# Performance work log

Hardware: AMD Instinct MI355X
Metric: run time of the kernel (lower is better)

## Reference

```python
import jax, jax.numpy as jnp
import numpy as np

B, D, L = 16, 256, 200
T = 1000   # max_frame_length
K = 3      # kernel_size
DW, DC = 4, 2


def setup_inputs() -> dict:
    key = jax.random.key(0)
    ks = jax.random.split(key, 16)
    plen = jax.random.randint(ks[0], (B,), 150, L + 1)
    pm = jnp.arange(L)[None, :] < plen[:, None]              # (B,L) True=valid
    phoneme_mask = pm[:, None, :]                            # (B,1,L)
    durations = jax.random.uniform(ks[1], (B, L), minval=1.0, maxval=8.0) * pm
    phoneme = jax.random.normal(ks[2], (B, D, L), dtype=jnp.float32)
    s = 0.05
    params = {
        'Wpw': jax.random.normal(ks[3], (D, D)) * s, 'bpw': jnp.zeros((D,)),
        'Cw': jax.random.normal(ks[4], (8, D, K)) * s, 'cbw': jnp.zeros((8,)),
        'Mw': jax.random.normal(ks[5], (10, DW)) * s, 'mbw': jnp.zeros((DW,)),
        'Lw': jax.random.normal(ks[6], (DW * D, D)) * s, 'lbw': jnp.zeros((D,)),
        'Wpc': jax.random.normal(ks[7], (D, D)) * s, 'bpc': jnp.zeros((D,)),
        'Cc': jax.random.normal(ks[8], (8, D, K)) * s, 'cbc': jnp.zeros((8,)),
        'Mc': jax.random.normal(ks[9], (10, DC)) * s, 'mbc': jnp.zeros((DC,)),
        'Lc': jax.random.normal(ks[10], (DW * DC, D)) * s, 'lbc': jnp.zeros((D,)),
        'Wo': jax.random.normal(ks[11], (D, 2 * D)) * s, 'bo': jnp.zeros((2 * D,)),
    }
    return {'durations': durations, 'phoneme': phoneme, 'phoneme_mask': phoneme_mask, **params}


def _conv_swish(x, W1, b1, Ck, cb, pm):
    # 1x1 conv (proj) then kernel-K 'same' conv then SiLU; mask padded phones
    h = jnp.einsum('od,bdl->bol', W1, x) + b1[None, :, None]
    h = jax.lax.conv_general_dilated(h, Ck, (1,), 'SAME',
                                     dimension_numbers=('NCH', 'OIH', 'NCH')) + cb[None, :, None]
    h = jax.nn.silu(h)
    h = jnp.where(pm[:, None, :], h, 0.0)
    return h.transpose(0, 2, 1)  # (B, L, 8)


def _mlp(S, E, h, M, mb):
    # concat start/end boundary scalars with per-phone conv features -> (B,T,L,10)
    feat = jnp.concatenate([S[..., None], E[..., None],
                            jnp.broadcast_to(h[:, None], (B, T, L, 8))], axis=-1)
    return jax.nn.silu(feat @ M + mb)


def _forward(durations, phoneme, phoneme_mask, Wpw, bpw, Cw, cbw, Mw, mbw, Lw, lbw,
             Wpc, bpc, Cc, cbc, Mc, mbc, Lc, lbc, Wo, bo):
    pm = phoneme_mask[:, 0, :]                                          # (B,L)
    frame_lengths = jnp.clip(jnp.round(durations.sum(-1)).astype(jnp.int32), 0, T)
    frame_mask = jnp.arange(T)[None, :] < frame_lengths[:, None]        # (B,T)
    attn_mask = frame_mask[:, :, None] & pm[:, None, :]                 # (B,T,L)
    sd = jnp.cumsum(durations, axis=-1)                                 # (B,L)
    sk = sd - durations
    t = jnp.arange(1, T + 1, dtype=durations.dtype)
    S = jnp.where(attn_mask, t[None, :, None] - sk[:, None, :], 0.0)    # (B,T,L)
    E = jnp.where(attn_mask, (sd - sk)[:, None, :], 0.0)                # (B,T,L)

    h_w = _conv_swish(phoneme, Wpw, bpw, Cw, cbw, pm)
    w = _mlp(S, E, h_w, Mw, mbw)                                        # (B,T,L,DW)
    w = jnp.where(pm[:, None, :, None], w, -jnp.inf)
    w = jax.nn.softmax(w, axis=2)                                       # softmax over phones
    w = jnp.where(frame_mask[:, :, None, None], w, 0.0)

    h_c = _conv_swish(phoneme, Wpc, bpc, Cc, cbc, pm)
    c = _mlp(S, E, h_c, Mc, mbc)                                        # (B,T,L,DC)

    wh = jnp.einsum('btlq,bdl->btqd', w, phoneme).reshape(B, T, DW * D) @ Lw + lbw
    wc = jnp.einsum('btlq,btlp->btqp', w, c).reshape(B, T, DW * DC) @ Lc + lbc
    whc = jnp.where(frame_mask[..., None], wh + wc, 0.0)                # (B,T,D)
    out = (whc @ Wo + bo).transpose(0, 2, 1)                            # (B,2D,T)
    return out, frame_mask, frame_lengths, w.transpose(0, 3, 1, 2)


def reference(durations, phoneme, phoneme_mask, Wpw, bpw, Cw, cbw, Mw, mbw, Lw, lbw,
              Wpc, bpc, Cc, cbc, Mc, mbc, Lc, lbc, Wo, bo):
    out, frame_mask, frame_lengths, w = _forward(
        durations, phoneme, phoneme_mask, Wpw, bpw, Cw, cbw, Mw, mbw, Lw, lbw,
        Wpc, bpc, Cc, cbc, Mc, mbc, Lc, lbc, Wo, bo)
    mean, log_std = jnp.split(out, 2, axis=1)                           # (B,D,T) each
    return (mean, log_std, frame_mask, frame_lengths, w)
```

## Files before the change

kernel.cpp:

```cpp
#include <hip/hip_runtime.h>
#include <hip/hip_bf16.h>
#include <math.h>

#define NB 16
#define ND 256
#define NL 200
#define NT 1000

typedef unsigned short ushort_t;
typedef __bf16 bf16x8 __attribute__((ext_vector_type(8)));
typedef float f32x4 __attribute__((ext_vector_type(4)));

#define OFF_FL    4981936u
#define OFF_GT    11535552u
#define OFF_WOT   15221952u
#define OFF_BASE  15287488u

__device__ __forceinline__ float silu_f(float x){ return x / (1.f + __expf(-x)); }
__device__ __forceinline__ ushort_t f2bf(float x){
  __hip_bfloat16 h = __float2bfloat16(x);
  return *(ushort_t*)&h;
}

__global__ __launch_bounds__(256, 2) void k_A(
    const float* __restrict__ dur, const float* __restrict__ ph,
    const float* __restrict__ Wp_w, const float* __restrict__ C_w, const float* __restrict__ bp_w,
    const float* __restrict__ Wp_c, const float* __restrict__ C_c, const float* __restrict__ bp_c,
    const float* __restrict__ Wo, const float* __restrict__ Lw,
    const float* __restrict__ cbw, const float* __restrict__ cbc,
    const float* __restrict__ Mw, const float* __restrict__ mbw,
    const float* __restrict__ Mc, const float* __restrict__ mbc,
    int* __restrict__ fl_ws, float* __restrict__ o_fm, float* __restrict__ o_fl,
    ushort_t* __restrict__ WoT, float4* __restrict__ base,
    ushort_t* __restrict__ Gt)
{
  __shared__ __align__(16) unsigned char smem[69632];
  int bid = blockIdx.x, tid = threadIdx.x;

  if (bid < 256){
    int r = bid;
    int b = r >> 4, x = r & 15;
    if (x >= 13){
      int l0 = 208 + (x - 13)*16;
      if (tid < 32)
        base[((size_t)(b*256 + l0 + (tid >> 1)))*2 + (tid & 1)] = make_float4(0,0,0,0);
      return;
    }
    float* sdur = (float*)smem;
    float* ssk  = sdur + 256;
    float (*phs)[256] = (float (*)[256])(ssk + 256);
    float (*Uw)[20] = (float (*)[20])((float*)phs + 18*256);
    float (*Uc)[20] = Uw + 256;
    float (*sh)[17] = (float (*)[17])((float*)Uc + 256*20);
    int l0 = x*16;

    if (tid < NL) sdur[tid] = dur[b*NL + tid];
    __syncthreads();
    if (tid == 0){
      float run = 0.f;
      for (int l = 0; l < NL; ++l){ ssk[l] = run; run += sdur[l]; }
    }
    {
      int d = tid;
      const float* pr = ph + ((size_t)b*ND + d)*NL;
      #pragma unroll
      for (int j = 0; j < 18; ++j){
        int l = l0 - 1 + j;
        phs[j][d] = (l >= 0 && l < NL) ? pr[l] : 0.f;
      }
    }
    __syncthreads();
    {
      int i = tid;
      float uw[18], uc[18];
      float bw = bp_w[i], bc = bp_c[i];
      #pragma unroll
      for (int j = 0; j < 18; ++j){ uw[j] = bw; uc[j] = bc; }
      const float4* wr = (const float4*)(Wp_w + (size_t)i*ND);
      const float4* cr = (const float4*)(Wp_c + (size_t)i*ND);
      for (int d4 = 0; d4 < 64; ++d4){
        float4 a = wr[d4], c = cr[d4];
        #pragma unroll
        for (int j = 0; j < 18; ++j){
          float4 p = *(const float4*)&phs[j][d4*4];
          uw[j] += a.x*p.x + a.y*p.y + a.z*p.z + a.w*p.w;
          uc[j] += c.x*p.x + c.y*p.y + c.z*p.z + c.w*p.w;
        }
      }
      #pragma unroll
      for (int j = 0; j < 18; ++j){
        int l = l0 - 1 + j;
        bool pad = (l < 0 || l >= NL);
        Uw[i][j] = pad ? 0.f : uw[j];
        Uc[i][j] = pad ? 0.f : uc[j];
      }
    }
    __syncthreads();
    {
      int lu = tid >> 4, u = tid & 15;
      int l = l0 + lu;
      float h = 0.f;
      if (l < NL){
        int branch = u >> 3, oc = u & 7;
        float (*U)[20] = branch ? Uc : Uw;
        const float* C = branch ? C_c : C_w;
        float val = (branch ? cbc : cbw)[oc];
        #pragma unroll 4
        for (int i = 0; i < ND; ++i){
          const float* cc = C + ((size_t)oc*ND + i)*3;
          val += cc[0]*U[i][lu] + cc[1]*U[i][lu + 1] + cc[2]*U[i][lu + 2];
        }
        float pm = (sdur[l] > 0.5f) ? 1.f : 0.f;
        h = silu_f(val) * pm;
      }
      sh[lu][u] = h;
    }
    __syncthreads();
    if (tid < 16){
      int ll = x*16 + tid;
      float4 o0 = make_float4(0,0,0,0);
      float4 o1 = make_float4(0,0,0,0);
      if (ll < NL){
        float dl  = sdur[ll];
        float pm  = (dl > 0.5f) ? 1.f : 0.f;
        float skl = ssk[ll];
        float c1[4], c2[2];
        #pragma unroll
        for (int q = 0; q < 4; ++q) c1[q] = mbw[q] + dl*Mw[4 + q] - skl*Mw[q];
        #pragma unroll
        for (int p = 0; p < 2; ++p) c2[p] = mbc[p] + dl*Mc[2 + p] - skl*Mc[p];
        #pragma unroll
        for (int j = 0; j < 8; ++j){
          float hwv = sh[tid][j], hcv = sh[tid][8 + j];
          #pragma unroll
          for (int q = 0; q < 4; ++q) c1[q] += hwv*Mw[(2 + j)*4 + q];
          #pragma unroll
          for (int p = 0; p < 2; ++p) c2[p] += hcv*Mc[(2 + j)*2 + p];
        }
        o0 = make_float4(c1[0], c1[1], c1[2], c1[3]);
        o1 = make_float4(c2[0], c2[1], pm, 0.f);
      }
      base[((size_t)(b*256 + ll))*2 + 0] = o0;
      base[((size_t)(b*256 + ll))*2 + 1] = o1;
    }
  } else if (bid < 512){
    int r = bid - 256;
    int xb = r & 1, yb = (r >> 1) & 1, bq = r >> 2;
    int b = bq >> 2, q = bq & 3;
    int m0 = yb * 128;
    int n0 = xb * 128;
    int lane = tid & 63, wave = tid >> 6;
    int wm = wave >> 1, wn = wave & 1;
    int col = lane & 15, kg4 = lane >> 4;
    ushort_t (*Asub)[136] = (ushort_t (*)[136])smem;
    ushort_t (*Bsub)[136] = (ushort_t (*)[136])(smem + 34816);
    int na = lane*2;

    f32x4 acc[4][4] = {};
    for (int kh = 0; kh < 2; ++kh){
      int d0 = kh*128;
      for (int rep = 0; rep < 32; ++rep){
        int dk = wave*32 + rep;
        float2 v = *(const float2*)(Lw + ((size_t)(q*256 + d0 + dk))*ND + m0 + na);
        Asub[na    ][dk] = f2bf(v.x);
        Asub[na + 1][dk] = f2bf(v.y);
      }
      for (int rep = 0; rep < 32; ++rep){
        int dk = wave*32 + rep;
        int l = n0 + na;
        float2 v; v.x = 0.f; v.y = 0.f;
        if (l < NL)
          v = *(const float2*)(ph + ((size_t)b*ND + d0 + dk)*NL + l);
        Bsub[na    ][dk] = f2bf(v.x);
        Bsub[na + 1][dk] = f2bf(v.y);
      }
      __syncthreads();
      for (int kt = 0; kt < 4; ++kt){
        int k0 = kt*32;
        bf16x8 afr[4], bfr[4];
        #pragma unroll
        for (int i = 0; i < 4; ++i)
          afr[i] = *(const bf16x8*)&Asub[wm*64 + i*16 + col][k0 + kg4*8];
        #pragma unroll
        for (int j = 0; j < 4; ++j)
          bfr[j] = *(const bf16x8*)&Bsub[wn*64 + j*16 + col][k0 + kg4*8];
        #pragma unroll
        for (int i = 0; i < 4; ++i)
          #pragma unroll
          for (int j = 0; j < 4; ++j)
            acc[i][j] = __builtin_amdgcn_mfma_f32_16x16x32_bf16(afr[i], bfr[j], acc[i][j], 0, 0, 0);
      }
      __syncthreads();
    }
    ushort_t (*st2)[136] = Asub;
    int rq = lane >> 4;
    #pragma unroll
    for (int i = 0; i < 4; ++i){
      #pragma unroll
      for (int rr = 0; rr < 4; ++rr){
        int rl = wm*64 + i*16 + rq*4 + rr;
        #pragma unroll
        for (int j = 0; j < 4; ++j){
          int cl = wn*64 + j*16 + col;
          st2[rl][cl] = f2bf(acc[i][j][rr]);
        }
      }
    }
    __syncthreads();
    #pragma unroll
    for (int rep = 0; rep < 8; ++rep){
      int row = rep*16 + (tid >> 4);
      int ch  = tid & 15;
      int l   = n0 + ch*8;
      if (l < NL){
        int n = m0 + row;
        *(uint4*)(Gt + ((size_t)(b*ND + n))*800 + q*NL + l) = *(const uint4*)&st2[row][ch*8];
      }
    }
  } else if (bid < 528){
    int b = bid - 512;
    float* sdur = (float*)smem;
    int* sfl = (int*)(sdur + 256);
    if (tid < NL) sdur[tid] = dur[b*NL + tid];
    __syncthreads();
    if (tid == 0){
      float run = 0.f;
      for (int l = 0; l < NL; ++l) run += sdur[l];
      int fl = (int)rintf(run);
      fl = fl < 0 ? 0 : (fl > NT ? NT : fl);
      sfl[0] = fl; fl_ws[b] = fl; o_fl[b] = (float)fl;
    }
    __syncthreads();
    int flv = sfl[0];
    for (int t = tid; t < NT; t += 256) o_fm[b*NT + t] = (t < flv) ? 1.f : 0.f;
  } else {
    int base_id = (bid - 528)*256 + tid;
    #pragma unroll
    for (int rep = 0; rep < 4; ++rep){
      int gid = rep*32768 + base_id;
      int n = gid >> 8, k = gid & 255;
      WoT[gid] = f2bf(Wo[(size_t)k*512 + n]);
    }
  }
}

#define AP 808
#define TT 64
__global__ __launch_bounds__(1024, 4) void k_wv_fused(
    const float4* __restrict__ base,
    const int* __restrict__ fl_ws,
    const float* __restrict__ Mw, const float* __restrict__ Mc,
    const ushort_t* __restrict__ Gt,
    const float* __restrict__ Lc,
    const float* __restrict__ lbc,
    const float* __restrict__ lbw,
    const ushort_t* __restrict__ WoT,
    const float* __restrict__ bo,
    float* __restrict__ wout,
    float* __restrict__ o_mean, float* __restrict__ o_lstd)
{
  __shared__ ushort_t As[TT*AP];
  __shared__ float    wcs[TT][8];
  int b = blockIdx.x;
  int m0 = blockIdx.y * TT;
  int tid = threadIdx.x, lane = tid & 63, wave = tid >> 6;
  int col = lane & 15, kg4 = lane >> 4;
  int fl = fl_ws[b];

  if (fl <= m0){
    for (int idx = tid; idx < TT*4*50; idx += 1024){
      int tl = idx / 200;
      int rqs = idx - tl*200;
      int q = rqs / 50, seg = rqs - q*50;
      int t = m0 + tl;
      if (t < NT)
        *(float4*)&wout[(((size_t)(b*4 + q))*NT + t)*NL + seg*4] = make_float4(0,0,0,0);
    }
    for (int idx = tid; idx < 512*16; idx += 1024){
      int s = idx >> 4, j = idx & 15;
      int t0 = m0 + j*4;
      if (t0 + 3 < NT){
        float v = bo[s];
        float4 v4 = make_float4(v, v, v, v);
        if (s < ND) *(float4*)&o_mean[((size_t)b*ND + s)*NT + t0] = v4;
        else        *(float4*)&o_lstd[((size_t)b*ND + (s - ND))*NT + t0] = v4;
      }
    }
    return;
  }

  int l0 = lane*4;
  bool lv = (l0 < NL);

  #pragma unroll
  for (int s = 0; s < 4; ++s){
    int tl = wave*4 + s, t = m0 + tl;
    if (t < fl) continue;
    for (int k = l0; k < 800; k += 256){
      uint2 zz2; zz2.x = 0u; zz2.y = 0u;
      *(uint2*)&As[tl*AP + k] = zz2;
    }
    if (lane < 8) wcs[tl][lane] = 0.f;
    if (t < NT && lv){
      float4 z4 = make_float4(0,0,0,0);
      #pragma unroll
      for (int q = 0; q < 4; ++q)
        *(float4*)&wout[(((size_t)(b*4 + q))*NT + t)*NL + l0] = z4;
    }
  }

  float b0a[4][4], b1x[4], b1y[4], pmv[4];
  #pragma unroll
  for (int e = 0; e < 4; ++e){
    float4 v0 = make_float4(0,0,0,0), v1 = make_float4(0,0,0,0);
    if (lv){
      v0 = base[((size_t)(b*256 + l0 + e))*2 + 0];
      v1 = base[((size_t)(b*256 + l0 + e))*2 + 1];
    }
    b0a[e][0] = v0.x; b0a[e][1] = v0.y; b0a[e][2] = v0.z; b0a[e][3] = v0.w;
    b1x[e] = v1.x; b1y[e] = v1.y; pmv[e] = v1.z;
  }
  float mwq[4] = {Mw[0], Mw[1], Mw[2], Mw[3]};
  float mcp[2] = {Mc[0], Mc[1]};

  for (int sp = 0; sp < 2; ++sp){
    int tl0 = wave*4 + sp*2;
    int t0 = m0 + tl0;
    if (t0 >= fl) break;
    bool a1 = (t0 + 1 < fl);
    float tf[2] = {(float)(t0 + 1), (float)(t0 + 2)};

    float z[2][4][4], mx[2][4];
    #pragma unroll
    for (int u = 0; u < 2; ++u)
      #pragma unroll
      for (int q = 0; q < 4; ++q) mx[u][q] = -INFINITY;
    #pragma unroll
    for (int e = 0; e < 4; ++e){
      #pragma unroll
      for (int u = 0; u < 2; ++u){
        #pragma unroll
        for (int q = 0; q < 4; ++q){
          float sv = silu_f(b0a[e][q] + tf[u]*mwq[q]);
          float zv = (pmv[e] > 0.f) ? sv : -INFINITY;
          z[u][e][q] = zv;
          mx[u][q] = fmaxf(mx[u][q], zv);
        }
      }
    }
    #pragma unroll
    for (int u = 0; u < 2; ++u)
      #pragma unroll
      for (int q = 0; q < 4; ++q){
        float v = mx[u][q];
        #pragma unroll
        for (int off = 32; off; off >>= 1) v = fmaxf(v, __shfl_xor(v, off));
        mx[u][q] = v;
      }
    float is4[2][4] = {{0,0,0,0},{0,0,0,0}};
    #pragma unroll
    for (int e = 0; e < 4; ++e){
      #pragma unroll
      for (int u = 0; u < 2; ++u){
        #pragma unroll
        for (int q = 0; q < 4; ++q){
          float ev = (pmv[e] > 0.f) ? __expf(z[u][e][q] - mx[u][q]) : 0.f;
          z[u][e][q] = ev;
          is4[u][q] += ev;
        }
      }
    }
    #pragma unroll
    for (int u = 0; u < 2; ++u)
      #pragma unroll
      for (int q = 0; q < 4; ++q){
        float v = is4[u][q];
        #pragma unroll
        for (int off = 32; off; off >>= 1) v += __shfl_xor(v, off);
        is4[u][q] = 1.f / v;
      }
    float cv[2][4][2];
    #pragma unroll
    for (int e = 0; e < 4; ++e)
      #pragma unroll
      for (int u = 0; u < 2; ++u){
        cv[u][e][0] = silu_f(b1x[e] + tf[u]*mcp[0]);
        cv[u][e][1] = silu_f(b1y[e] + tf[u]*mcp[1]);
      }
    float wc[2][8];
    #pragma unroll
    for (int u = 0; u < 2; ++u)
      #pragma unroll
      for (int x = 0; x < 8; ++x) wc[u][x] = 0.f;
    #pragma unroll
    for (int u = 0; u < 2; ++u){
      bool act = (u == 0) || a1;
      int t = t0 + u, tl = tl0 + u;
      #pragma unroll
      for (int q = 0; q < 4; ++q){
        float w0 = z[u][0][q]*is4[u][q];
        float w1 = z[u][1][q]*is4[u][q];
        float w2 = z[u][2][q]*is4[u][q];
        float w3 = z[u][3][q]*is4[u][q];
        if (act && lv){
          *(float4*)&wout[(((size_t)(b*4 + q))*NT + t)*NL + l0] =
              make_float4(w0, w1, w2, w3);
          uint2 pk;
          pk.x = (unsigned)f2bf(w0) | ((unsigned)f2bf(w1) << 16);
          pk.y = (unsigned)f2bf(w2) | ((unsigned)f2bf(w3) << 16);
          *(uint2*)&As[tl*AP + q*NL + l0] = pk;
        }
        wc[u][q*2 + 0] += w0*cv[u][0][0] + w1*cv[u][1][0] + w2*cv[u][2][0] + w3*cv[u][3][0];
        wc[u][q*2 + 1] += w0*cv[u][0][1] + w1*cv[u][1][1] + w2*cv[u][2][1] + w3*cv[u][3][1];
      }
    }
    #pragma unroll
    for (int u = 0; u < 2; ++u){
      if (u == 1 && !a1) break;
      #pragma unroll
      for (int x = 0; x < 8; ++x){
        float v = wc[u][x];
        #pragma unroll
        for (int off = 32; off; off >>= 1) v += __shfl_xor(v, off);
        wc[u][x] = v;
      }
      if (lane == 0){
        #pragma unroll
        for (int x = 0; x < 8; ++x) wcs[tl0 + u][x] = wc[u][x];
      }
    }
  }
  __syncthreads();

  f32x4 acc[4] = {};
  const ushort_t* Gb = Gt + (size_t)b*ND*800;
  for (int kt = 0; kt < 25; ++kt){
    int k0 = kt*32;
    bf16x8 afr[4], bfr;
    #pragma unroll
    for (int i = 0; i < 4; ++i)
      afr[i] = *(const bf16x8*)(&As[(i*16 + col)*AP + k0 + kg4*8]);
    bfr = *(const bf16x8*)(Gb + ((size_t)(wave*16 + col))*800 + k0 + kg4*8);
    #pragma unroll
    for (int i = 0; i < 4; ++i)
      acc[i] = __builtin_amdgcn_mfma_f32_16x16x32_bf16(afr[i], bfr, acc[i], 0, 0, 0);
  }
  __syncthreads();

  ushort_t (*stc)[264] = (ushort_t (*)[264])As;
  {
    int rq = lane >> 4;
    int n = wave*16 + col;
    float lbn = lbc[n], lbwn = lbw[n];
    float lcn[8];
    #pragma unroll
    for (int u = 0; u < 8; ++u) lcn[u] = Lc[u*ND + n];
    #pragma unroll
    for (int i = 0; i < 4; ++i){
      #pragma unroll
      for (int r = 0; r < 4; ++r){
        int tl = i*16 + rq*4 + r;
        int t = m0 + tl;
        if (t < NT){
          float f = (t < fl) ? 1.f : 0.f;
          float vcv = lbn
            + wcs[tl][0]*lcn[0] + wcs[tl][1]*lcn[1]
            + wcs[tl][2]*lcn[2] + wcs[tl][3]*lcn[3]
            + wcs[tl][4]*lcn[4] + wcs[tl][5]*lcn[5]
            + wcs[tl][6]*lcn[6] + wcs[tl][7]*lcn[7];
          stc[tl][n] = f2bf(f * (acc[i][r] + lbwn + vcv));
        }
      }
    }
  }
  __syncthreads();

  {
    f32x4 acc2[2][4] = {};
    for (int kt = 0; kt < 8; ++kt){
      int k0 = kt*32;
      bf16x8 afr[2], bfr[4];
      #pragma unroll
      for (int j = 0; j < 4; ++j)
        bfr[j] = *(const bf16x8*)(&stc[j*16 + col][k0 + kg4*8]);
      #pragma unroll
      for (int i = 0; i < 2; ++i)
        afr[i] = *(const bf16x8*)(WoT + ((size_t)(wave*32 + i*16 + col))*ND + k0 + kg4*8);
      #pragma unroll
      for (int i = 0; i < 2; ++i)
        #pragma unroll
        for (int j = 0; j < 4; ++j)
          acc2[i][j] = __builtin_amdgcn_mfma_f32_16x16x32_bf16(afr[i], bfr[j], acc2[i][j], 0, 0, 0);
    }
    int rq = lane >> 4;
    #pragma unroll
    for (int i = 0; i < 2; ++i){
      #pragma unroll
      for (int r = 0; r < 4; ++r){
        int s = wave*32 + i*16 + rq*4 + r;
        float bov = bo[s];
        #pragma unroll
        for (int j = 0; j < 4; ++j){
          int t = m0 + j*16 + col;
          if (t < NT){
            float v = acc2[i][j][r] + bov;
            if (s < ND) o_mean[((size_t)b*ND + s)*NT + t] = v;
            else        o_lstd[((size_t)b*ND + (s - ND))*NT + t] = v;
          }
        }
      }
    }
  }
}

extern "C" void kernel_launch(void* const* d_in, const int* in_sizes, int n_in,
                              void* d_out, int out_size, void* d_ws, size_t ws_size,
                              hipStream_t stream)
{
  const float* dur = (const float*)d_in[0];
  const float* ph  = (const float*)d_in[1];
  const float* Wpw = (const float*)d_in[3];
  const float* bpw = (const float*)d_in[4];
  const float* Cw  = (const float*)d_in[5];
  const float* cbw = (const float*)d_in[6];
  const float* Mw  = (const float*)d_in[7];
  const float* mbw = (const float*)d_in[8];
  const float* Lw  = (const float*)d_in[9];
  const float* lbw = (const float*)d_in[10];
  const float* Wpc = (const float*)d_in[11];
  const float* bpc = (const float*)d_in[12];
  const float* Cc  = (const float*)d_in[13];
  const float* cbc = (const float*)d_in[14];
  const float* Mc  = (const float*)d_in[15];
  const float* mbc = (const float*)d_in[16];
  const float* Lc  = (const float*)d_in[17];
  const float* lbc = (const float*)d_in[18];
  const float* Wo  = (const float*)d_in[19];
  const float* bo  = (const float*)d_in[20];

  float* out    = (float*)d_out;
  float* o_mean = out;
  float* o_lstd = out + (size_t)NB*ND*NT;
  float* o_fm   = o_lstd + (size_t)NB*ND*NT;
  float* o_fl   = o_fm + NB*NT;
  float* o_w    = o_fl + NB;

  float* ws   = (float*)d_ws;
  int*   fl   = (int*)(ws + OFF_FL);
  ushort_t* Gt   = (ushort_t*)(ws + OFF_GT);
  ushort_t* WoT  = (ushort_t*)(ws + OFF_WOT);
  float4*   base = (float4*)(ws + OFF_BASE);

  k_A<<<656, 256, 0, stream>>>(dur, ph, Wpw, Cw, bpw, Wpc, Cc, bpc, Wo, Lw,
                               cbw, cbc, Mw, mbw, Mc, mbc,
                               fl, o_fm, o_fl, WoT, base, Gt);
  {
    dim3 g(NB, 16);
    k_wv_fused<<<g, 1024, 0, stream>>>(base, fl, Mw, Mc, Gt, Lc, lbc, lbw,
                                       WoT, bo, o_w, o_mean, o_lstd);
  }
}
```

Before: 239.4 us.

## Shrink k_A shared memory and raise occupancy by serializing branch projections

Cuts k_A's static shared memory from about 68KB to about 39KB and raises launch bounds to 4 blocks per SM. The w and c projection/conv branches now run one after the other, reusing a single U buffer. The MFMA path stages K in 64-wide chunks instead of 128. The aim is more resident blocks to hide latency, paid for with extra synchronisations, serialized branch work, and tighter register limits that may cause spills.

Measured after the change: 256.5 us. +7.2%, slower.

```diff
diff --git a/kernel.cpp b/kernel.cpp
--- a/kernel.cpp
+++ b/kernel.cpp
@@ -22,7 +22,7 @@
   return *(ushort_t*)&h;
 }
 
-__global__ __launch_bounds__(256, 2) void k_A(
+__global__ __launch_bounds__(256, 4) void k_A(
     const float* __restrict__ dur, const float* __restrict__ ph,
     const float* __restrict__ Wp_w, const float* __restrict__ C_w, const float* __restrict__ bp_w,
     const float* __restrict__ Wp_c, const float* __restrict__ C_c, const float* __restrict__ bp_c,
@@ -34,26 +34,26 @@
     ushort_t* __restrict__ WoT, float4* __restrict__ base,
     ushort_t* __restrict__ Gt)
 {
-  __shared__ __align__(16) unsigned char smem[69632];
+  __shared__ __align__(16) unsigned char smem[39936];
   int bid = blockIdx.x, tid = threadIdx.x;
 
   if (bid < 256){
-    int r = bid;
-    int b = r >> 4, x = r & 15;
+    int b = bid >> 4, x = bid & 15;
     if (x >= 13){
       int l0 = 208 + (x - 13)*16;
       if (tid < 32)
         base[((size_t)(b*256 + l0 + (tid >> 1)))*2 + (tid & 1)] = make_float4(0,0,0,0);
       return;
     }
-    float* sdur = (float*)smem;
-    float* ssk  = sdur + 256;
-    float (*phs)[256] = (float (*)[256])(ssk + 256);
-    float (*Uw)[20] = (float (*)[20])((float*)phs + 18*256);
-    float (*Uc)[20] = Uw + 256;
-    float (*sh)[17] = (float (*)[17])((float*)Uc + 256*20);
+    float* phs  = (float*)smem;
+    float* U    = (float*)(smem + 18432);
+    float* ssk  = (float*)(smem + 36864);
+    float (*sh)[16] = (float (*)[16])(smem + 37888);
+    float* sdur = (float*)(smem + 38912);
     int l0 = x*16;
 
+    sdur[tid & 255] = 0.f;
+    __syncthreads();
     if (tid < NL) sdur[tid] = dur[b*NL + tid];
     __syncthreads();
     if (tid == 0){
@@ -61,61 +61,60 @@
       for (int l = 0; l < NL; ++l){ ssk[l] = run; run += sdur[l]; }
     }
     {
-      int d = tid;
-      const float* pr = ph + ((size_t)b*ND + d)*NL;
+      const float* pr = ph + ((size_t)b*ND + tid)*NL;
       #pragma unroll
       for (int j = 0; j < 18; ++j){
         int l = l0 - 1 + j;
-        phs[j][d] = (l >= 0 && l < NL) ? pr[l] : 0.f;
+        phs[j*256 + tid] = (l >= 0 && l < NL) ? pr[l] : 0.f;
       }
     }
     __syncthreads();
-    {
-      int i = tid;
-      float uw[18], uc[18];
-      float bw = bp_w[i], bc = bp_c[i];
-      #pragma unroll
-      for (int j = 0; j < 18; ++j){ uw[j] = bw; uc[j] = bc; }
-      const float4* wr = (const float4*)(Wp_w + (size_t)i*ND);
-      const float4* cr = (const float4*)(Wp_c + (size_t)i*ND);
-      for (int d4 = 0; d4 < 64; ++d4){
-        float4 a = wr[d4], c = cr[d4];
+
+    for (int br = 0; br < 2; ++br){
+      const float* Wp  = br ? Wp_c : Wp_w;
+      const float* bpv = br ? bp_c : bp_w;
+      {
+        int i = tid;
+        float u[18];
+        float bb = bpv[i];
+        #pragma unroll
+        for (int j = 0; j < 18; ++j) u[j] = bb;
+        const float4* wr = (const float4*)(Wp + (size_t)i*ND);
+        for (int d4 = 0; d4 < 64; ++d4){
+          float4 a = wr[d4];
+          #pragma unroll
+          for (int j = 0; j < 18; ++j){
+            float4 p = *(const float4*)&phs[j*256 + d4*4];
+            u[j] += a.x*p.x + a.y*p.y + a.z*p.z + a.w*p.w;
+          }
+        }
         #pragma unroll
         for (int j = 0; j < 18; ++j){
-          float4 p = *(const float4*)&phs[j][d4*4];
-          uw[j] += a.x*p.x + a.y*p.y + a.z*p.z + a.w*p.w;
-          uc[j] += c.x*p.x + c.y*p.y + c.z*p.z + c.w*p.w;
-        }
-      }
-      #pragma unroll
-      for (int j = 0; j < 18; ++j){
-        int l = l0 - 1 + j;
-        bool pad = (l < 0 || l >= NL);
-        Uw[i][j] = pad ? 0.f : uw[j];
-        Uc[i][j] = pad ? 0.f : uc[j];
-      }
-    }
-    __syncthreads();
-    {
-      int lu = tid >> 4, u = tid & 15;
-      int l = l0 + lu;
-      float h = 0.f;
-      if (l < NL){
-        int branch = u >> 3, oc = u & 7;
-        float (*U)[20] = branch ? Uc : Uw;
-        const float* C = branch ? C_c : C_w;
-        float val = (branch ? cbc : cbw)[oc];
-        #pragma unroll 4
-        for (int i = 0; i < ND; ++i){
-          const float* cc = C + ((size_t)oc*ND + i)*3;
-          val += cc[0]*U[i][lu] + cc[1]*U[i][lu + 1] + cc[2]*U[i][lu + 2];
-        }
-        float pm = (sdur[l] > 0.5f) ? 1.f : 0.f;
-        h = silu_f(val) * pm;
-      }
-      sh[lu][u] = h;
-    }
-    __syncthreads();
+          int l = l0 - 1 + j;
+          bool pad = (l < 0 || l >= NL);
+          U[i*18 + j] = pad ? 0.f : u[j];
+        }
+      }
+      __syncthreads();
+      if (tid < 128){
+        int lu = tid >> 3, oc = tid & 7;
+        int l = l0 + lu;
+        float h = 0.f;
+        if (l < NL){
+          const float* C = br ? C_c : C_w;
+          float val = (br ? cbc : cbw)[oc];
+          #pragma unroll 4
+          for (int i = 0; i < ND; ++i){
+            const float* cc = C + ((size_t)oc*ND + i)*3;
+            val += cc[0]*U[i*18 + lu] + cc[1]*U[i*18 + lu + 1] + cc[2]*U[i*18 + lu + 2];
+          }
+          float pm = (sdur[l] > 0.5f) ? 1.f : 0.f;
+          h = silu_f(val) * pm;
+        }
+        sh[lu][br*8 + oc] = h;
+      }
+      __syncthreads();
+    }
     if (tid < 16){
       int ll = x*16 + tid;
       float4 o0 = make_float4(0,0,0,0);
@@ -152,21 +151,21 @@
     int lane = tid & 63, wave = tid >> 6;
     int wm = wave >> 1, wn = wave & 1;
     int col = lane & 15, kg4 = lane >> 4;
-    ushort_t (*Asub)[136] = (ushort_t (*)[136])smem;
-    ushort_t (*Bsub)[136] = (ushort_t (*)[136])(smem + 34816);
+    ushort_t (*Asub)[72] = (ushort_t (*)[72])smem;
+    ushort_t (*Bsub)[72] = (ushort_t (*)[72])(smem + 18432);
     int na = lane*2;
 
     f32x4 acc[4][4] = {};
-    for (int kh = 0; kh < 2; ++kh){
-      int d0 = kh*128;
-      for (int rep = 0; rep < 32; ++rep){
-        int dk = wave*32 + rep;
+    for (int kq = 0; kq < 4; ++kq){
+      int d0 = kq*64;
+      for (int rep = 0; rep < 16; ++rep){
+        int dk = wave*16 + rep;
         float2 v = *(const float2*)(Lw + ((size_t)(q*256 + d0 + dk))*ND + m0 + na);
         Asub[na    ][dk] = f2bf(v.x);
         Asub[na + 1][dk] = f2bf(v.y);
       }
-      for (int rep = 0; rep < 32; ++rep){
-        int dk = wave*32 + rep;
+      for (int rep = 0; rep < 16; ++rep){
+        int dk = wave*16 + rep;
         int l = n0 + na;
         float2 v; v.x = 0.f; v.y = 0.f;
         if (l < NL)
@@ -175,7 +174,7 @@
         Bsub[na + 1][dk] = f2bf(v.y);
       }
       __syncthreads();
-      for (int kt = 0; kt < 4; ++kt){
+      for (int kt = 0; kt < 2; ++kt){
         int k0 = kt*32;
         bf16x8 afr[4], bfr[4];
         #pragma unroll
@@ -192,7 +191,7 @@
       }
       __syncthreads();
     }
-    ushort_t (*st2)[136] = Asub;
+    ushort_t (*st2)[136] = (ushort_t (*)[136])smem;
     int rq = lane >> 4;
     #pragma unroll
     for (int i = 0; i < 4; ++i){
```
